# Optimization experiments

Measured on AMD Instinct MI355X. Metric: run time of the kernel, lower is better.

The kernel has to match this reference:

```python
import jax, jax.numpy as jnp
import numpy as np

NUM_HEADS = 4
KERNEL = 7
DILATION = 1
EMBED = 128
CTX = 256
RANK = 8
HEAD_DIM = EMBED // NUM_HEADS
SCALE = HEAD_DIM ** (-0.5)


def setup_inputs() -> dict:
    key = jax.random.key(0)
    ks = jax.random.split(key, 16)
    B, H, W = 4, 64, 64
    inp = {
        "x": jax.random.normal(ks[0], (B, H, W, EMBED), jnp.float32),
        "context": jax.random.normal(ks[1], (B, CTX), jnp.float32),
        # base QKV linear (torch Linear: y = x @ W.T + b)
        "Wqkv": jax.random.normal(ks[2], (3 * EMBED, EMBED), jnp.float32) * 0.02,
        "bqkv": jax.random.normal(ks[3], (3 * EMBED,), jnp.float32) * 0.02,
        # bilinear LoRA params (init scale 0.01 as in source)
        "A": jax.random.normal(ks[4], (EMBED, RANK), jnp.float32) * 0.01,
        "Blora": jax.random.normal(ks[5], (CTX, RANK), jnp.float32) * 0.01,
        "Vlora": jax.random.normal(ks[6], (3 * EMBED, RANK), jnp.float32) * 0.01,
        # gate MLP: Linear(ctx,16) -> ReLU -> Linear(16,1) -> Sigmoid
        "g1w": jax.random.normal(ks[7], (16, CTX), jnp.float32) * 0.05,
        "g1b": jnp.zeros((16,), jnp.float32),
        "g2w": jnp.full((1, 16), -5.0, jnp.float32) * 0.0 + jax.random.normal(ks[8], (1, 16), jnp.float32) * 0.01 - 5.0 / 16.0,
        "g2b": jnp.full((1,), -5.0, jnp.float32),
        # output projection
        "Wproj": jax.random.normal(ks[9], (EMBED, EMBED), jnp.float32) * 0.02,
        "bproj": jnp.zeros((EMBED,), jnp.float32),
    }
    return inp


def _windows(t, H, W):
    # t: [B, nh, H+2p, W+2p, d] -> [B, nh, H, W, K^2, d]
    ws = []
    for i in range(KERNEL):
        for j in range(KERNEL):
            ws.append(t[:, :, i * DILATION:i * DILATION + H, j * DILATION:j * DILATION + W, :])
    return jnp.stack(ws, axis=4)


def reference(x, context, Wqkv, bqkv, A, Blora, Vlora, g1w, g1b, g2w, g2b, Wproj, bproj):
    B, H, W, C = x.shape
    nh, hd = NUM_HEADS, HEAD_DIM
    # context-modulated QKV: base + alpha * ((xA) * (cB)) V^T
    base = x @ Wqkv.T + bqkv                                   # [B,H,W,3C]
    c_proj = context @ Blora                                   # [B,r]
    delta = ((x @ A) * c_proj[:, None, None, :]) @ Vlora.T     # [B,H,W,3C]
    alpha = jax.nn.sigmoid(jax.nn.relu(context @ g1w.T + g1b) @ g2w.T + g2b)  # [B,1]
    qkv = base + alpha[:, None, None, :] * delta               # [B,H,W,3C]

    qkv = qkv.reshape(B, H, W, 3, nh, hd)
    qkv = jnp.transpose(qkv, (3, 0, 4, 1, 2, 5))               # [3,B,nh,H,W,hd]
    q, k, v = qkv[0], qkv[1], qkv[2]

    pad = DILATION * (KERNEL - 1) // 2
    pw = ((0, 0), (0, 0), (pad, pad), (pad, pad), (0, 0))
    k_p = jnp.pad(k, pw)
    v_p = jnp.pad(v, pw)
    kw = _windows(k_p, H, W)                                   # [B,nh,H,W,K2,hd]
    vw = _windows(v_p, H, W)

    attn = jnp.einsum('bnijd,bnijkd->bnijk', q, kw) * SCALE    # [B,nh,H,W,K2]
    attn = jax.nn.softmax(attn, axis=-1)
    out = jnp.einsum('bnijk,bnijkd->bnijd', attn, vw)          # [B,nh,H,W,hd]

    out = jnp.transpose(out, (0, 2, 3, 1, 4)).reshape(B, H, W, C)
    out = out @ Wproj.T + bproj
    return out
```

## Files before the change

### kernel.cpp

```cpp
#include <hip/hip_runtime.h>
#include <cstddef>

#define CTXDIM 256
#define RANK 8
#define KW 7
#define SCALE 0.17677669529663687f
#define NPIX 16384
#define PLANE16 (NPIX * 128)
#define AH 14
#define ANH 196
#define KST 40
#define WSTRIDE 136

typedef _Float16 half8 __attribute__((ext_vector_type(8)));
typedef _Float16 half2_t __attribute__((ext_vector_type(2)));
typedef float floatx4 __attribute__((ext_vector_type(4)));

#if defined(__has_builtin)
#if __has_builtin(__builtin_amdgcn_fdot2)
#define HAVE_FDOT2 1
#endif
#endif

struct Params {
  const float *x, *ctx, *Wqkv, *bqkv, *A, *Blora, *Vlora;
  const float *g1w, *g1b, *g2w, *g2b, *Wproj, *bproj;
  float* out;
  _Float16* qkv16;
  _Float16* at16;
};

__device__ __forceinline__ void compute_cal(const Params& p, int tid,
                                            float* cal_s) {
  const int b = tid >> 6, lane = tid & 63;
  const float c0 = p.ctx[b * CTXDIM + lane];
  const float c1 = p.ctx[b * CTXDIM + 64 + lane];
  const float c2 = p.ctx[b * CTXDIM + 128 + lane];
  const float c3 = p.ctx[b * CTXDIM + 192 + lane];
  float cp[RANK];
#pragma unroll
  for (int r = 0; r < RANK; ++r) {
    float q = c0 * p.Blora[lane * RANK + r] + c1 * p.Blora[(64 + lane) * RANK + r] +
              c2 * p.Blora[(128 + lane) * RANK + r] + c3 * p.Blora[(192 + lane) * RANK + r];
#pragma unroll
    for (int s = 32; s; s >>= 1) q += __shfl_xor(q, s, 64);
    cp[r] = q;
  }
  float gacc = 0.f;
#pragma unroll
  for (int h = 0; h < 16; ++h) {
    float q = c0 * p.g1w[h * CTXDIM + lane] + c1 * p.g1w[h * CTXDIM + 64 + lane] +
              c2 * p.g1w[h * CTXDIM + 128 + lane] + c3 * p.g1w[h * CTXDIM + 192 + lane];
#pragma unroll
    for (int s = 32; s; s >>= 1) q += __shfl_xor(q, s, 64);
    gacc += fmaxf(q + p.g1b[h], 0.f) * p.g2w[h];
  }
  if (lane == 0) {
    const float alpha = 1.f / (1.f + __expf(-(gacc + p.g2b[0])));
#pragma unroll
    for (int r = 0; r < RANK; ++r) cal_s[b * RANK + r] = alpha * cp[r];
  }
}

__device__ __forceinline__ void stage_rows_f16(const float* __restrict__ src,
                                               _Float16* dst, int tid) {
  const int row = tid >> 2;
  const int c0 = (tid & 3) * 32;
  const float* sp = src + (size_t)row * 128 + c0;
  _Float16* dp = dst + row * WSTRIDE + c0;
#pragma unroll
  for (int i = 0; i < 4; ++i) {
    const float4 a = *(const float4*)(sp + i * 8);
    const float4 b = *(const float4*)(sp + i * 8 + 4);
    half8 o;
    o[0] = (_Float16)a.x; o[1] = (_Float16)a.y;
    o[2] = (_Float16)a.z; o[3] = (_Float16)a.w;
    o[4] = (_Float16)b.x; o[5] = (_Float16)b.y;
    o[6] = (_Float16)b.z; o[7] = (_Float16)b.w;
    *(half8*)(dp + i * 8) = o;
  }
}

__global__ __launch_bounds__(256) void gemm1_kernel(Params p) {
  __shared__ __align__(16) _Float16 xs[64 * WSTRIDE];
  __shared__ __align__(16) _Float16 wsh[64 * WSTRIDE];
  __shared__ float cal_s[32];
  const int tid = threadIdx.x;
  const int bx = blockIdx.x, byg = blockIdx.y, z = blockIdx.z;
  const int m0 = z * 4096 + bx * 64;

  compute_cal(p, tid, cal_s);
  stage_rows_f16(p.x + (size_t)m0 * 128, xs, tid);
  __syncthreads();

  const int lane = tid & 63;
  const int w = tid >> 6;
  const int r = lane & 15;
  const int quad = lane >> 4;
  const int k = tid & 127;
  const int hgrp = tid >> 7;
  const float4 a0 = *(const float4*)&p.A[k * RANK];
  const float4 a1 = *(const float4*)&p.A[k * RANK + 4];
  const float* cb = &cal_s[z * RANK];
  const float c0 = cb[0], c1 = cb[1], c2 = cb[2], c3 = cb[3];
  const float c4 = cb[4], c5 = cb[5], c6 = cb[6], c7 = cb[7];

  for (int i = 0; i < 3; ++i) {
    const int n0 = (byg * 3 + i) * 64;

#pragma unroll
    for (int rr = 0; rr < 32; ++rr) {
      const int row = hgrp * 32 + rr;
      const int o = n0 + row;
      const float4 v0 = *(const float4*)&p.Vlora[o * RANK];
      const float4 v1 = *(const float4*)&p.Vlora[o * RANK + 4];
      float d = a0.x * v0.x * c0;
      d = fmaf(a0.y * v0.y, c1, d);
      d = fmaf(a0.z * v0.z, c2, d);
      d = fmaf(a0.w * v0.w, c3, d);
      d = fmaf(a1.x * v1.x, c4, d);
      d = fmaf(a1.y * v1.y, c5, d);
      d = fmaf(a1.z * v1.z, c6, d);
      d = fmaf(a1.w * v1.w, c7, d);
      wsh[row * WSTRIDE + k] = (_Float16)(p.Wqkv[o * 128 + k] + d);
    }
    __syncthreads();

    const _Float16* ap = xs + (w * 16 + r) * WSTRIDE + quad * 8;
    const _Float16* bp = wsh + r * WSTRIDE + quad * 8;
    floatx4 acc0 = {0.f, 0.f, 0.f, 0.f};
    floatx4 acc1 = acc0, acc2 = acc0, acc3 = acc0;
#pragma unroll
    for (int kc = 0; kc < 4; ++kc) {
      const half8 a  = *(const half8*)(ap + kc * 32);
      const half8 b0 = *(const half8*)(bp + kc * 32);
      const half8 b1 = *(const half8*)(bp + 16 * WSTRIDE + kc * 32);
      const half8 b2 = *(const half8*)(bp + 32 * WSTRIDE + kc * 32);
      const half8 b3 = *(const half8*)(bp + 48 * WSTRIDE + kc * 32);
      acc0 = __builtin_amdgcn_mfma_f32_16x16x32_f16(a, b0, acc0, 0, 0, 0);
      acc1 = __builtin_amdgcn_mfma_f32_16x16x32_f16(a, b1, acc1, 0, 0, 0);
      acc2 = __builtin_amdgcn_mfma_f32_16x16x32_f16(a, b2, acc2, 0, 0, 0);
      acc3 = __builtin_amdgcn_mfma_f32_16x16x32_f16(a, b3, acc3, 0, 0, 0);
    }

    const int mbase = m0 + w * 16 + quad * 4;
    floatx4 accs[4] = {acc0, acc1, acc2, acc3};
#pragma unroll
    for (int nt = 0; nt < 4; ++nt) {
      const int ncol = n0 + nt * 16 + r;
      const float bv = p.bqkv[ncol];
      _Float16* cp = p.qkv16 + (size_t)(ncol >> 7) * PLANE16 +
                     (size_t)mbase * 128 + (ncol & 127);
#pragma unroll
      for (int reg = 0; reg < 4; ++reg)
        cp[(size_t)reg * 128] = (_Float16)(accs[nt][reg] + bv);
    }
    if (i != 2) __syncthreads();
  }
}

__global__ __launch_bounds__(256) void attn_kernel(Params p) {
  __shared__ __align__(16) _Float16 ks16[ANH * KST];
  __shared__ __align__(16) _Float16 vs16[ANH * KST];

  const int bid = blockIdx.x;
  const int h  = bid & 3;
  const int tj = (bid >> 2) & 7;
  const int ti = (bid >> 5) & 7;
  const int b  = bid >> 8;
  const int tid = threadIdx.x;

  const _Float16* kpl = p.qkv16 + PLANE16;
  const _Float16* vpl = p.qkv16 + 2 * (size_t)PLANE16;

  const int pix = tid >> 2;
  const int qtr = tid & 3;
  const int pi = pix >> 3;
  const int pj = pix & 7;
  const int n = b * 4096 + (ti * 8 + pi) * 64 + tj * 8 + pj;
  const int dbase = qtr * 8;
  const half8 q0 = *(const half8*)(p.qkv16 + (size_t)n * 128 + h * 32 + dbase);

  const int i0 = ti * 8 - 3;
  const int j0 = tj * 8 - 3;
#pragma unroll
  for (int it = 0; it < 4; ++it) {
    const int s = tid + it * 256;
    if (s < ANH * 4) {
      const int pp = s >> 2;
      const int d8 = (s & 3) * 8;
      const int hr = pp / AH;
      const int hc = pp - hr * AH;
      const int ii = i0 + hr;
      const int jj = j0 + hc;
      half8 kv = {0, 0, 0, 0, 0, 0, 0, 0};
      half8 vv = {0, 0, 0, 0, 0, 0, 0, 0};
      if ((unsigned)ii < 64u && (unsigned)jj < 64u) {
        const size_t g = (size_t)(b * 4096 + ii * 64 + jj) * 128 + h * 32 + d8;
        kv = *(const half8*)(kpl + g);
        vv = *(const half8*)(vpl + g);
      }
      *(half8*)&ks16[pp * KST + d8] = kv;
      *(half8*)&vs16[pp * KST + d8] = vv;
    }
  }
  __syncthreads();

  float l[49];
  float mx = -1e30f;
#pragma unroll
  for (int di = 0; di < KW; ++di) {
#pragma unroll
    for (int dj = 0; dj < KW; ++dj) {
      const int hp = (pi + di) * AH + (pj + dj);
      const half8 k0 = *(const half8*)&ks16[hp * KST + dbase];
      float pr = 0.f;
#ifdef HAVE_FDOT2
#pragma unroll
      for (int e = 0; e < 4; ++e) {
        half2_t qa = {q0[2 * e], q0[2 * e + 1]};
        half2_t ka = {k0[2 * e], k0[2 * e + 1]};
        pr = __builtin_amdgcn_fdot2(qa, ka, pr, false);
      }
#else
#pragma unroll
      for (int e = 0; e < 8; ++e)
        pr = fmaf((float)q0[e], (float)k0[e], pr);
#endif
      pr += __shfl_xor(pr, 1, 64);
      pr += __shfl_xor(pr, 2, 64);
      const float lv = pr * SCALE;
      l[di * KW + dj] = lv;
      mx = fmaxf(mx, lv);
    }
  }

  float sum = 0.f;
#pragma unroll
  for (int s = 0; s < 49; ++s) {
    const float w = __expf(l[s] - mx);
    l[s] = w;
    sum += w;
  }
  const float inv = 1.f / sum;

  float o[8];
#pragma unroll
  for (int e = 0; e < 8; ++e) o[e] = 0.f;
#pragma unroll
  for (int di = 0; di < KW; ++di) {
#pragma unroll
    for (int dj = 0; dj < KW; ++dj) {
      const int hp = (pi + di) * AH + (pj + dj);
      const float w = l[di * KW + dj];
      const half8 v0 = *(const half8*)&vs16[hp * KST + dbase];
#pragma unroll
      for (int e = 0; e < 8; ++e)
        o[e] = fmaf(w, (float)v0[e], o[e]);
    }
  }

  half8 r0;
#pragma unroll
  for (int e = 0; e < 8; ++e) r0[e] = (_Float16)(o[e] * inv);
  *(half8*)(p.at16 + (size_t)n * 128 + h * 32 + dbase) = r0;
}

__global__ __launch_bounds__(256) void gemm2_kernel(Params p) {
  __shared__ __align__(16) _Float16 wsh[64 * WSTRIDE];
  const int tid = threadIdx.x;
  const int m0 = blockIdx.x * 64;
  const int n0 = blockIdx.y * 64;

  stage_rows_f16(p.Wproj + (size_t)n0 * 128, wsh, tid);
  __syncthreads();

  const int lane = tid & 63;
  const int w = tid >> 6;
  const int r = lane & 15;
  const int quad = lane >> 4;
  const _Float16* ap = p.at16 + (size_t)(m0 + w * 16 + r) * 128 + quad * 8;
  const _Float16* bp = wsh + r * WSTRIDE + quad * 8;

  floatx4 acc0 = {0.f, 0.f, 0.f, 0.f};
  floatx4 acc1 = acc0, acc2 = acc0, acc3 = acc0;
#pragma unroll
  for (int kc = 0; kc < 4; ++kc) {
    const half8 a  = *(const half8*)(ap + kc * 32);
    const half8 b0 = *(const half8*)(bp + kc * 32);
    const half8 b1 = *(const half8*)(bp + 16 * WSTRIDE + kc * 32);
    const half8 b2 = *(const half8*)(bp + 32 * WSTRIDE + kc * 32);
    const half8 b3 = *(const half8*)(bp + 48 * WSTRIDE + kc * 32);
    acc0 = __builtin_amdgcn_mfma_f32_16x16x32_f16(a, b0, acc0, 0, 0, 0);
    acc1 = __builtin_amdgcn_mfma_f32_16x16x32_f16(a, b1, acc1, 0, 0, 0);
    acc2 = __builtin_amdgcn_mfma_f32_16x16x32_f16(a, b2, acc2, 0, 0, 0);
    acc3 = __builtin_amdgcn_mfma_f32_16x16x32_f16(a, b3, acc3, 0, 0, 0);
  }

  const int mbase = m0 + w * 16 + quad * 4;
  floatx4 accs[4] = {acc0, acc1, acc2, acc3};
#pragma unroll
  for (int nt = 0; nt < 4; ++nt) {
    const int n = n0 + nt * 16 + r;
    const float bv = p.bproj[n];
    float* cp = p.out + (size_t)mbase * 128 + n;
#pragma unroll
    for (int reg = 0; reg < 4; ++reg)
      cp[(size_t)reg * 128] = accs[nt][reg] + bv;
  }
}

extern "C" void kernel_launch(void* const* d_in, const int* in_sizes, int n_in,
                              void* d_out, int out_size, void* d_ws, size_t ws_size,
                              hipStream_t stream) {
  char* ws = (char*)d_ws;
  Params hp;
  hp.x     = (const float*)d_in[0];
  hp.ctx   = (const float*)d_in[1];
  hp.Wqkv  = (const float*)d_in[2];
  hp.bqkv  = (const float*)d_in[3];
  hp.A     = (const float*)d_in[4];
  hp.Blora = (const float*)d_in[5];
  hp.Vlora = (const float*)d_in[6];
  hp.g1w   = (const float*)d_in[7];
  hp.g1b   = (const float*)d_in[8];
  hp.g2w   = (const float*)d_in[9];
  hp.g2b   = (const float*)d_in[10];
  hp.Wproj = (const float*)d_in[11];
  hp.bproj = (const float*)d_in[12];
  hp.out   = (float*)d_out;
  hp.qkv16 = (_Float16*)(ws + (1u << 20));
  hp.at16  = (_Float16*)(ws + (14u << 20));

  gemm1_kernel<<<dim3(64, 2, 4), 256, 0, stream>>>(hp);
  attn_kernel<<<1024, 256, 0, stream>>>(hp);
  gemm2_kernel<<<dim3(256, 2), 256, 0, stream>>>(hp);
}
```

Before: 58.20 us.

## Compute neighborhood attention tile with MFMA over masked halo window

Replaces the per-pixel scalar fdot2 neighborhood attention with MFMA 32x32x16 matrix ops. Each wave computes QK^T for 32 query pixels against a 160-row band of the 14x16 halo and masks out-of-window entries before softmax. The probabilities are repacked through lane shuffles into an A operand and multiplied by a transposed, swizzled V tile in shared memory. Blocks shrink to 128 threads. This trades dense-tile redundant compute (about 160 keys per query instead of 49) and a scalar transposed V store for matrix-core throughput.

```diff
diff --git a/kernel.cpp b/kernel.cpp
--- a/kernel.cpp
+++ b/kernel.cpp
@@ -7,20 +7,13 @@
 #define SCALE 0.17677669529663687f
 #define NPIX 16384
 #define PLANE16 (NPIX * 128)
-#define AH 14
-#define ANH 196
-#define KST 40
 #define WSTRIDE 136
 
 typedef _Float16 half8 __attribute__((ext_vector_type(8)));
 typedef _Float16 half2_t __attribute__((ext_vector_type(2)));
 typedef float floatx4 __attribute__((ext_vector_type(4)));
-
-#if defined(__has_builtin)
-#if __has_builtin(__builtin_amdgcn_fdot2)
-#define HAVE_FDOT2 1
-#endif
-#endif
+typedef float floatx16 __attribute__((ext_vector_type(16)));
+typedef int intx4 __attribute__((ext_vector_type(4)));
 
 struct Params {
   const float *x, *ctx, *Wqkv, *bqkv, *A, *Blora, *Vlora;
@@ -159,9 +152,117 @@
   }
 }
 
-__global__ __launch_bounds__(256) void attn_kernel(Params p) {
-  __shared__ __align__(16) _Float16 ks16[ANH * KST];
-  __shared__ __align__(16) _Float16 vs16[ANH * KST];
+__device__ __forceinline__ int vta(int d, int k) {
+  const int sig = (d + (d >> 3)) & 7;
+  return d * 256 + (((k >> 3) ^ sig) << 3) + (k & 7);
+}
+
+__device__ __forceinline__ int packh(float x, float y) {
+  half2_t h;
+  h[0] = (_Float16)x;
+  h[1] = (_Float16)y;
+  return __builtin_bit_cast(int, h);
+}
+
+template <int MT0, int W>
+__device__ __forceinline__ void attn_wave(const Params& p,
+                                          const _Float16* kls,
+                                          const _Float16* vtl,
+                                          half8 qb0, half8 qb1,
+                                          int m31, int l5, int pi, int pj,
+                                          int b, int ti, int tj, int h) {
+  const floatx16 zz = {0.f,0.f,0.f,0.f,0.f,0.f,0.f,0.f,
+                       0.f,0.f,0.f,0.f,0.f,0.f,0.f,0.f};
+  floatx16 acc[5];
+#pragma unroll
+  for (int mt = 0; mt < 5; ++mt) {
+    const int Mt = MT0 + mt;
+    const half8 ka0 = *(const half8*)&kls[(Mt * 32 + m31) * 40 + l5 * 8];
+    const half8 ka1 = *(const half8*)&kls[(Mt * 32 + m31) * 40 + 16 + l5 * 8];
+    floatx16 a = zz;
+    a = __builtin_amdgcn_mfma_f32_32x32x16_f16(ka0, qb0, a, 0, 0, 0);
+    a = __builtin_amdgcn_mfma_f32_32x32x16_f16(ka1, qb1, a, 0, 0, 0);
+    acc[mt] = a;
+  }
+
+  bool vR[14];
+#pragma unroll
+  for (int i = 0; i < 14; ++i) vR[i] = (unsigned)(i - pi) < 7u;
+  bool vC[8];
+#pragma unroll
+  for (int c8 = 0; c8 < 8; ++c8) {
+    const int hcv = (c8 & 3) + 8 * (c8 >> 2) + 4 * l5;
+    vC[c8] = (unsigned)(hcv - pj) < 7u;
+  }
+
+  float mxp[4] = {-1e30f, -1e30f, -1e30f, -1e30f};
+#pragma unroll
+  for (int mt = 0; mt < 5; ++mt) {
+#pragma unroll
+    for (int reg = 0; reg < 16; ++reg) {
+      const bool v = vR[2 * (MT0 + mt) + (reg >> 3)] &&
+                     vC[(reg & 3) + 4 * ((reg >> 2) & 1)];
+      const float x = v ? acc[mt][reg] : -1e30f;
+      acc[mt][reg] = x;
+      mxp[reg & 3] = fmaxf(mxp[reg & 3], x);
+    }
+  }
+  float mx = fmaxf(fmaxf(mxp[0], mxp[1]), fmaxf(mxp[2], mxp[3]));
+  mx = fmaxf(mx, __shfl_xor(mx, 32, 64));
+
+  const float SC2 = SCALE * 1.4426950408889634f;
+  float sp[4] = {0.f, 0.f, 0.f, 0.f};
+#pragma unroll
+  for (int mt = 0; mt < 5; ++mt) {
+#pragma unroll
+    for (int reg = 0; reg < 16; ++reg) {
+      const float pv = exp2f((acc[mt][reg] - mx) * SC2);
+      acc[mt][reg] = pv;
+      sp[reg & 3] += pv;
+    }
+  }
+  float sum = (sp[0] + sp[1]) + (sp[2] + sp[3]);
+  sum += __shfl_xor(sum, 32, 64);
+  const float inv = 1.f / sum;
+
+  floatx16 oacc = zz;
+  const int sigd = (m31 + (m31 >> 3)) & 7;
+  const int vbase = m31 * 256;
+#pragma unroll
+  for (int kk = 0; kk < 10; ++kk) {
+    const int ks = MT0 * 2 + kk;
+    const int mt = (ks >> 1) - MT0;
+    const int r8 = 8 * (ks & 1);
+    const int E00 = packh(acc[mt][r8 + 0] * inv, acc[mt][r8 + 1] * inv);
+    const int E01 = packh(acc[mt][r8 + 2] * inv, acc[mt][r8 + 3] * inv);
+    const int E10 = packh(acc[mt][r8 + 4] * inv, acc[mt][r8 + 5] * inv);
+    const int E11 = packh(acc[mt][r8 + 6] * inv, acc[mt][r8 + 7] * inv);
+    const int R00 = __shfl_xor(E00, 32, 64);
+    const int R01 = __shfl_xor(E01, 32, 64);
+    const int R10 = __shfl_xor(E10, 32, 64);
+    const int R11 = __shfl_xor(E11, 32, 64);
+    const int A0 = l5 ? R10 : E00;
+    const int A1 = l5 ? R11 : E01;
+    const int A2 = l5 ? E10 : R00;
+    const int A3 = l5 ? E11 : R01;
+    const intx4 ai = {A0, A1, A2, A3};
+    const half8 af = __builtin_bit_cast(half8, ai);
+    const half8 vb = *(const half8*)&vtl[vbase + (((2 * ks + l5) ^ sigd) << 3)];
+    oacc = __builtin_amdgcn_mfma_f32_32x32x16_f16(af, vb, oacc, 0, 0, 0);
+  }
+
+#pragma unroll
+  for (int reg = 0; reg < 16; ++reg) {
+    const int rowM = (reg & 3) + 8 * (reg >> 2) + 4 * l5;
+    const int pxt = W * 32 + rowM;
+    const int n = b * 4096 + (ti * 8 + (pxt >> 3)) * 64 + tj * 8 + (pxt & 7);
+    p.at16[(size_t)n * 128 + h * 32 + m31] = (_Float16)oacc[reg];
+  }
+}
+
+__global__ __launch_bounds__(128, 2) void attn_kernel(Params p) {
+  __shared__ __align__(16) _Float16 kls[224 * 40];
+  __shared__ __align__(16) _Float16 vtl[32 * 256];
 
   const int bid = blockIdx.x;
   const int h  = bid & 3;
@@ -169,101 +270,55 @@
   const int ti = (bid >> 5) & 7;
   const int b  = bid >> 8;
   const int tid = threadIdx.x;
+  const int lane = tid & 63;
+  const int w = tid >> 6;
+  const int m31 = lane & 31;
+  const int l5 = lane >> 5;
 
   const _Float16* kpl = p.qkv16 + PLANE16;
   const _Float16* vpl = p.qkv16 + 2 * (size_t)PLANE16;
 
-  const int pix = tid >> 2;
-  const int qtr = tid & 3;
-  const int pi = pix >> 3;
-  const int pj = pix & 7;
-  const int n = b * 4096 + (ti * 8 + pi) * 64 + tj * 8 + pj;
-  const int dbase = qtr * 8;
-  const half8 q0 = *(const half8*)(p.qkv16 + (size_t)n * 128 + h * 32 + dbase);
+  const int pix = w * 32 + m31;
+  const int pi = pix >> 3, pj = pix & 7;
+  const int nq = b * 4096 + (ti * 8 + pi) * 64 + tj * 8 + pj;
+  const half8 qb0 = *(const half8*)(p.qkv16 + (size_t)nq * 128 + h * 32 + l5 * 8);
+  const half8 qb1 = *(const half8*)(p.qkv16 + (size_t)nq * 128 + h * 32 + 16 + l5 * 8);
+
+  for (int idx = tid; idx < 896; idx += 128) {
+    const int d = idx & 31;
+    const int kk = idx >> 5;
+    const int k = (kk >> 1) * 16 + 14 + (kk & 1);
+    vtl[vta(d, k)] = (_Float16)0.f;
+  }
 
   const int i0 = ti * 8 - 3;
   const int j0 = tj * 8 - 3;
-#pragma unroll
-  for (int it = 0; it < 4; ++it) {
-    const int s = tid + it * 256;
-    if (s < ANH * 4) {
-      const int pp = s >> 2;
-      const int d8 = (s & 3) * 8;
-      const int hr = pp / AH;
-      const int hc = pp - hr * AH;
-      const int ii = i0 + hr;
-      const int jj = j0 + hc;
-      half8 kv = {0, 0, 0, 0, 0, 0, 0, 0};
-      half8 vv = {0, 0, 0, 0, 0, 0, 0, 0};
-      if ((unsigned)ii < 64u && (unsigned)jj < 64u) {
-        const size_t g = (size_t)(b * 4096 + ii * 64 + jj) * 128 + h * 32 + d8;
-        kv = *(const half8*)(kpl + g);
-        vv = *(const half8*)(vpl + g);
-      }
-      *(half8*)&ks16[pp * KST + d8] = kv;
-      *(half8*)&vs16[pp * KST + d8] = vv;
-    }
+  for (int s = tid; s < 784; s += 128) {
+    const int pp = s >> 2;
+    const int d8 = (s & 3) * 8;
+    const int hr = pp / 14;
+    const int hc = pp - hr * 14;
+    const int row = hr * 16 + hc;
+    const int ii = i0 + hr;
+    const int jj = j0 + hc;
+    half8 kv = {0, 0, 0, 0, 0, 0, 0, 0};
+    half8 vv = {0, 0, 0, 0, 0, 0, 0, 0};
+    if ((unsigned)ii < 64u && (unsigned)jj < 64u) {
+      const size_t g = (size_t)(b * 4096 + ii * 64 + jj) * 128 + h * 32 + d8;
+      kv = *(const half8*)(kpl + g);
+      vv = *(const half8*)(vpl + g);
+    }
+    *(half8*)&kls[row * 40 + d8] = kv;
+#pragma unroll
+    for (int e = 0; e < 8; ++e)
+      vtl[vta(d8 + e, row)] = vv[e];
   }
   __syncthreads();
 
-  float l[49];
-  float mx = -1e30f;
-#pragma unroll
-  for (int di = 0; di < KW; ++di) {
-#pragma unroll
-    for (int dj = 0; dj < KW; ++dj) {
-      const int hp = (pi + di) * AH + (pj + dj);
-      const half8 k0 = *(const half8*)&ks16[hp * KST + dbase];
-      float pr = 0.f;
-#ifdef HAVE_FDOT2
-#pragma unroll
-      for (int e = 0; e < 4; ++e) {
-        half2_t qa = {q0[2 * e], q0[2 * e + 1]};
-        half2_t ka = {k0[2 * e], k0[2 * e + 1]};
-        pr = __builtin_amdgcn_fdot2(qa, ka, pr, false);
-      }
-#else
-#pragma unroll
-      for (int e = 0; e < 8; ++e)
-        pr = fmaf((float)q0[e], (float)k0[e], pr);
-#endif
-      pr += __shfl_xor(pr, 1, 64);
-      pr += __shfl_xor(pr, 2, 64);
-      const float lv = pr * SCALE;
-      l[di * KW + dj] = lv;
-      mx = fmaxf(mx, lv);
-    }
-  }
-
-  float sum = 0.f;
-#pragma unroll
-  for (int s = 0; s < 49; ++s) {
-    const float w = __expf(l[s] - mx);
-    l[s] = w;
-    sum += w;
-  }
-  const float inv = 1.f / sum;
-
-  float o[8];
-#pragma unroll
-  for (int e = 0; e < 8; ++e) o[e] = 0.f;
-#pragma unroll
-  for (int di = 0; di < KW; ++di) {
-#pragma unroll
-    for (int dj = 0; dj < KW; ++dj) {
-      const int hp = (pi + di) * AH + (pj + dj);
-      const float w = l[di * KW + dj];
-      const half8 v0 = *(const half8*)&vs16[hp * KST + dbase];
-#pragma unroll
-      for (int e = 0; e < 8; ++e)
-        o[e] = fmaf(w, (float)v0[e], o[e]);
-    }
-  }
-
-  half8 r0;
-#pragma unroll
-  for (int e = 0; e < 8; ++e) r0[e] = (_Float16)(o[e] * inv);
-  *(half8*)(p.at16 + (size_t)n * 128 + h * 32 + dbase) = r0;
+  if (w == 0)
+    attn_wave<0, 0>(p, kls, vtl, qb0, qb1, m31, l5, pi, pj, b, ti, tj, h);
+  else
+    attn_wave<2, 1>(p, kls, vtl, qb0, qb1, m31, l5, pi, pj, b, ti, tj, h);
 }
 
 __global__ __launch_bounds__(256) void gemm2_kernel(Params p) {
@@ -333,6 +388,6 @@
   hp.at16  = (_Float16*)(ws + (14u << 20));
 
   gemm1_kernel<<<dim3(64, 2, 4), 256, 0, stream>>>(hp);
-  attn_kernel<<<1024, 256, 0, stream>>>(hp);
+  attn_kernel<<<1024, 128, 0, stream>>>(hp);
   gemm2_kernel<<<dim3(256, 2), 256, 0, stream>>>(hp);
 }
```

Result: faster. 50.24 us (-13.7%).
